# Performance work log

Hardware: AMD Instinct MI355X
Metric: run time of the kernel (lower is better)

The kernel has to match this reference:

```python
import jax, jax.numpy as jnp
import numpy as np

E, H, I, K, T = 32, 2048, 768, 4, 2048


def setup_inputs() -> dict:
    key = jax.random.key(0)
    k1, k2, k3, k4, k5 = jax.random.split(key, 5)
    hidden_states = jax.random.normal(k1, (T, H), dtype=jnp.float32)
    top_k_index = jax.random.randint(k2, (T, K), 0, E, dtype=jnp.int64)
    top_k_weights = jax.random.uniform(k3, (T, K), dtype=jnp.float32)
    gate_up_proj = jax.random.normal(k4, (E, H, 2 * I), dtype=jnp.float32) * 0.02
    down_proj = jax.random.normal(k5, (E, I, H), dtype=jnp.float32) * 0.02
    return {
        "hidden_states": hidden_states,
        "top_k_index": top_k_index,
        "top_k_weights": top_k_weights,
        "gate_up_proj": gate_up_proj,
        "down_proj": down_proj,
    }


def reference(hidden_states, top_k_index, top_k_weights, gate_up_proj, down_proj):
    # Dense routing-weight matrix [T, E]: zeros scattered with top-k weights
    num_tokens = hidden_states.shape[0]
    routing = jnp.zeros((num_tokens, E), dtype=hidden_states.dtype)
    routing = routing.at[jnp.arange(num_tokens)[:, None], top_k_index].set(top_k_weights)

    # Batched (grouped) GEMM over all experts; weights are stored transposed
    # gate_up_proj: [E, H, 2I] -> gu: [E, T, 2I]
    gu = jnp.einsum('th,ehi->eti', hidden_states, gate_up_proj)
    gate, up = jnp.split(gu, 2, axis=-1)           # each [E, T, I]
    inter = jax.nn.silu(gate) * up                 # [E, T, I]
    # down_proj: [E, I, H] -> per-expert output [E, T, H]
    expert_out = jnp.einsum('eti,eih->eth', inter, down_proj)
    # Weighted combine over experts
    out = jnp.einsum('te,eth->th', routing, expert_out)
    return out
```

## Files before the change

### kernel.cpp

```cpp
#include <hip/hip_runtime.h>
#include <hip/hip_bf16.h>

#define E_ 32
#define H_ 2048
#define I_ 768
#define T_ 2048
#define TWO_I 1536
#define MAX_TILES 96

typedef __attribute__((ext_vector_type(8))) short short8;
typedef __attribute__((ext_vector_type(4))) float floatx4;

#define WS_OFFSETS 0
#define WS_IDS     1024
#define WS_WTS     (1024 + 32768)
#define WS_TILES   (1024 + 65536)
#define WS_SLOTTJ  69632
#define WS_INTER   131072
#define WS_HID16   (131072 + 8192*768*2)
#define WS_EO      21102592ULL

__device__ __forceinline__ unsigned short f2bf(float f) {
  union { float f; unsigned u; } v; v.f = f;
  unsigned r = v.u + 0x7FFFu + ((v.u >> 16) & 1u);
  return (unsigned short)(r >> 16);
}

__device__ __forceinline__ unsigned pkbf(float a, float b) {
  __hip_bfloat162 h = __float22bfloat162_rn(float2{a, b});
  union { __hip_bfloat162 h; unsigned u; } v; v.h = h; return v.u;
}

__global__ void build_routing(const int* __restrict__ idx, const float* __restrict__ w,
                              char* __restrict__ ws) {
  int* offs = (int*)(ws + WS_OFFSETS);
  int* ids  = (int*)(ws + WS_IDS);
  float* wt = (float*)(ws + WS_WTS);
  int* tiles = (int*)(ws + WS_TILES);
  int* slot_tj = (int*)(ws + WS_SLOTTJ);
  __shared__ int s_cnt[E_];
  __shared__ int s_pos[E_];
  int tid = threadIdx.x;
  if (tid < E_) s_cnt[tid] = 0;
  __syncthreads();
  for (int i = tid; i < T_ * 4; i += 256) {
    int t = i >> 2, j = i & 3;
    int e = idx[i];
    bool keep = true;
    for (int j2 = j + 1; j2 < 4; ++j2) if (idx[t * 4 + j2] == e) keep = false;
    if (keep) atomicAdd(&s_cnt[e], 1);
  }
  __syncthreads();
  if (tid == 0) {
    int run = 0;
    for (int e = 0; e < E_; ++e) { offs[e] = run; s_pos[e] = run; run += s_cnt[e]; }
    offs[E_] = run;
    int nt = 0;
    for (int e = 0; e < E_; ++e)
      for (int m0 = 0; m0 < s_cnt[e]; m0 += 128) tiles[nt++] = (e << 16) | (m0 >> 7);
    for (; nt < MAX_TILES; ++nt) tiles[nt] = -1;
  }
  __syncthreads();
  for (int i = tid; i < T_ * 4; i += 256) {
    int t = i >> 2, j = i & 3;
    int e = idx[i];
    bool keep = true;
    for (int j2 = j + 1; j2 < 4; ++j2) if (idx[t * 4 + j2] == e) keep = false;
    if (keep) {
      int p = atomicAdd(&s_pos[e], 1);
      ids[p] = t;
      wt[p] = w[i];
      slot_tj[i] = p;
    } else {
      slot_tj[i] = -1;
    }
  }
}

__global__ void cvt_hidden(const float* __restrict__ hs, char* __restrict__ ws) {
  int g = blockIdx.x * 256 + threadIdx.x;
  const float4 f0 = ((const float4*)hs)[g * 2];
  const float4 f1 = ((const float4*)hs)[g * 2 + 1];
  uint4 o;
  o.x = pkbf(f0.x, f0.y); o.y = pkbf(f0.z, f0.w);
  o.z = pkbf(f1.x, f1.y); o.w = pkbf(f1.z, f1.w);
  ((uint4*)(ws + WS_HID16))[g] = o;
}

__global__ __launch_bounds__(256, 2) void gemm1(
    const float* __restrict__ gup, char* __restrict__ ws) {
  const int* offs = (const int*)(ws + WS_OFFSETS);
  const int* ids  = (const int*)(ws + WS_IDS);
  const int* tiles = (const int*)(ws + WS_TILES);
  const unsigned short* h16 = (const unsigned short*)(ws + WS_HID16);
  unsigned short* inter = (unsigned short*)(ws + WS_INTER);

  int tl = tiles[blockIdx.y];
  if (tl < 0) return;
  int e = tl >> 16, m0 = (tl & 0xffff) << 7;
  int start = offs[e];
  int mrem = offs[e + 1] - start - m0;
  int n0 = blockIdx.x * 64;

  __shared__ __align__(16) unsigned short Al[128][72];
  __shared__ __align__(16) unsigned short Bl[128][72];

  int tid = threadIdx.x, lane = tid & 63, wid = tid >> 6;
  int wy = wid >> 1, wx = wid & 1, quad = lane >> 4, l15 = lane & 15;

  floatx4 acc[4][4] = {};

  int arow[4], ako[4];
  const unsigned short* asrc[4];
#pragma unroll
  for (int u = 0; u < 4; ++u) {
    int lin = tid + u * 256;
    arow[u] = lin >> 3; ako[u] = (lin & 7) * 8;
    int tok = (arow[u] < mrem) ? ids[start + m0 + arow[u]] : -1;
    asrc[u] = (tok >= 0) ? h16 + (size_t)tok * H_ + ako[u] : nullptr;
  }
  const float* gB[4];
  int brow0[4], bofs[4];
#pragma unroll
  for (int pp = 0; pp < 4; ++pp) {
    int lin2 = tid + 256 * pp;
    int k2 = lin2 >> 5, c4 = lin2 & 31;
    int gcol = (c4 < 16) ? (n0 + c4 * 4) : (I_ + n0 + (c4 - 16) * 4);
    gB[pp] = gup + (size_t)e * H_ * TWO_I + (size_t)(2 * k2) * TWO_I + gcol;
    brow0[pp] = c4 * 4;
    int chunkp = (k2 >> 2) ^ (c4 & 7);
    bofs[pp] = chunkp * 8 + (k2 & 3) * 2;
  }

  uint4 pf_a[4];
  float4 pf0[4], pf1[4];

  auto loadA = [&](int kb) {
#pragma unroll
    for (int u = 0; u < 4; ++u)
      pf_a[u] = asrc[u] ? *(const uint4*)(asrc[u] + (size_t)kb * 64) : uint4{0u, 0u, 0u, 0u};
  };
  auto loadB = [&](int kb) {
#pragma unroll
    for (int pp = 0; pp < 4; ++pp) {
      const float* p = gB[pp] + (size_t)kb * 64 * TWO_I;
      pf0[pp] = *(const float4*)p;
      pf1[pp] = *(const float4*)(p + TWO_I);
    }
  };

  loadA(0); loadB(0);
  for (int kb = 0; kb < H_ / 64; ++kb) {
#pragma unroll
    for (int u = 0; u < 4; ++u) *(uint4*)&Al[arow[u]][ako[u]] = pf_a[u];
#pragma unroll
    for (int pp = 0; pp < 4; ++pp) {
      *(unsigned*)&Bl[brow0[pp] + 0][bofs[pp]] = pkbf(pf0[pp].x, pf1[pp].x);
      *(unsigned*)&Bl[brow0[pp] + 1][bofs[pp]] = pkbf(pf0[pp].y, pf1[pp].y);
      *(unsigned*)&Bl[brow0[pp] + 2][bofs[pp]] = pkbf(pf0[pp].z, pf1[pp].z);
      *(unsigned*)&Bl[brow0[pp] + 3][bofs[pp]] = pkbf(pf0[pp].w, pf1[pp].w);
    }
    __syncthreads();
    if (kb + 1 < H_ / 64) { loadA(kb + 1); loadB(kb + 1); }
#pragma unroll
    for (int ks = 0; ks < 2; ++ks) {
      short8 af[4], bfr[4];
#pragma unroll
      for (int mi = 0; mi < 4; ++mi)
        af[mi] = *(const short8*)&Al[wy * 64 + mi * 16 + l15][ks * 32 + quad * 8];
#pragma unroll
      for (int ni = 0; ni < 4; ++ni) {
        int j = (ni < 2) ? (wx * 32 + ni * 16 + l15) : (64 + wx * 32 + (ni - 2) * 16 + l15);
        int ch = (ks * 4 + quad) ^ ((j >> 2) & 7);
        bfr[ni] = *(const short8*)&Bl[j][ch * 8];
      }
#pragma unroll
      for (int mi = 0; mi < 4; ++mi)
#pragma unroll
        for (int ni = 0; ni < 4; ++ni)
          acc[mi][ni] = __builtin_amdgcn_mfma_f32_16x16x32_bf16(af[mi], bfr[ni], acc[mi][ni], 0, 0, 0);
    }
    __syncthreads();
  }

#pragma unroll
  for (int mi = 0; mi < 4; ++mi) {
#pragma unroll
    for (int r = 0; r < 4; ++r) {
      int row = wy * 64 + mi * 16 + quad * 4 + r;
      if (row < mrem) {
        int slot = start + m0 + row;
#pragma unroll
        for (int ni = 0; ni < 2; ++ni) {
          float g = acc[mi][ni][r];
          float u = acc[mi][ni + 2][r];
          float s = g / (1.f + __expf(-g));
          int col = n0 + wx * 32 + ni * 16 + l15;
          inter[(size_t)slot * I_ + col] = f2bf(s * u);
        }
      }
    }
  }
}

__global__ __launch_bounds__(256, 2) void gemm2(
    const float* __restrict__ down, char* __restrict__ ws) {
  const int* offs = (const int*)(ws + WS_OFFSETS);
  const float* wt = (const float*)(ws + WS_WTS);
  const int* tiles = (const int*)(ws + WS_TILES);
  const unsigned short* inter = (const unsigned short*)(ws + WS_INTER);
  float* eo = (float*)(ws + WS_EO);

  int tl = tiles[blockIdx.y];
  if (tl < 0) return;
  int e = tl >> 16, m0 = (tl & 0xffff) << 7;
  int start = offs[e];
  int mrem = offs[e + 1] - start - m0;
  int n0 = blockIdx.x * 128;

  __shared__ __align__(16) unsigned short Al[128][72];
  __shared__ __align__(16) unsigned short Bl[128][72];

  int tid = threadIdx.x, lane = tid & 63, wid = tid >> 6;
  int wy = wid >> 1, wx = wid & 1, quad = lane >> 4, l15 = lane & 15;

  floatx4 acc[4][4] = {};

  int arow[4], ako[4];
  const unsigned short* asrc[4];
#pragma unroll
  for (int u = 0; u < 4; ++u) {
    int lin = tid + u * 256;
    arow[u] = lin >> 3; ako[u] = (lin & 7) * 8;
    asrc[u] = (arow[u] < mrem) ? inter + (size_t)(start + m0 + arow[u]) * I_ + ako[u] : nullptr;
  }
  const float* gB[4];
  int brow0[4], bofs[4];
#pragma unroll
  for (int pp = 0; pp < 4; ++pp) {
    int lin2 = tid + 256 * pp;
    int k2 = lin2 >> 5, c4 = lin2 & 31;
    gB[pp] = down + (size_t)e * I_ * H_ + (size_t)(2 * k2) * H_ + (n0 + c4 * 4);
    brow0[pp] = c4 * 4;
    int chunkp = (k2 >> 2) ^ (c4 & 7);
    bofs[pp] = chunkp * 8 + (k2 & 3) * 2;
  }

  uint4 pf_a[4];
  float4 pf0[4], pf1[4];

  auto loadA = [&](int kb) {
#pragma unroll
    for (int u = 0; u < 4; ++u)
      pf_a[u] = asrc[u] ? *(const uint4*)(asrc[u] + (size_t)kb * 64) : uint4{0u, 0u, 0u, 0u};
  };
  auto loadB = [&](int kb) {
#pragma unroll
    for (int pp = 0; pp < 4; ++pp) {
      const float* p = gB[pp] + (size_t)kb * 64 * H_;
      pf0[pp] = *(const float4*)p;
      pf1[pp] = *(const float4*)(p + H_);
    }
  };

  loadA(0); loadB(0);
  for (int kb = 0; kb < I_ / 64; ++kb) {
#pragma unroll
    for (int u = 0; u < 4; ++u) *(uint4*)&Al[arow[u]][ako[u]] = pf_a[u];
#pragma unroll
    for (int pp = 0; pp < 4; ++pp) {
      *(unsigned*)&Bl[brow0[pp] + 0][bofs[pp]] = pkbf(pf0[pp].x, pf1[pp].x);
      *(unsigned*)&Bl[brow0[pp] + 1][bofs[pp]] = pkbf(pf0[pp].y, pf1[pp].y);
      *(unsigned*)&Bl[brow0[pp] + 2][bofs[pp]] = pkbf(pf0[pp].z, pf1[pp].z);
      *(unsigned*)&Bl[brow0[pp] + 3][bofs[pp]] = pkbf(pf0[pp].w, pf1[pp].w);
    }
    __syncthreads();
    if (kb + 1 < I_ / 64) { loadA(kb + 1); loadB(kb + 1); }
#pragma unroll
    for (int ks = 0; ks < 2; ++ks) {
      short8 af[4], bfr[4];
#pragma unroll
      for (int mi = 0; mi < 4; ++mi)
        af[mi] = *(const short8*)&Al[wy * 64 + mi * 16 + l15][ks * 32 + quad * 8];
#pragma unroll
      for (int ni = 0; ni < 4; ++ni) {
        int j = wx * 64 + ni * 16 + l15;
        int ch = (ks * 4 + quad) ^ ((j >> 2) & 7);
        bfr[ni] = *(const short8*)&Bl[j][ch * 8];
      }
#pragma unroll
      for (int mi = 0; mi < 4; ++mi)
#pragma unroll
        for (int ni = 0; ni < 4; ++ni)
          acc[mi][ni] = __builtin_amdgcn_mfma_f32_16x16x32_bf16(af[mi], bfr[ni], acc[mi][ni], 0, 0, 0);
    }
    __syncthreads();
  }

#pragma unroll
  for (int mi = 0; mi < 4; ++mi) {
#pragma unroll
    for (int r = 0; r < 4; ++r) {
      int row = wy * 64 + mi * 16 + quad * 4 + r;
      if (row < mrem) {
        int slot = start + m0 + row;
        float wv = wt[slot];
#pragma unroll
        for (int ni = 0; ni < 4; ++ni) {
          int col = n0 + wx * 64 + ni * 16 + l15;
          eo[(size_t)slot * H_ + col] = wv * acc[mi][ni][r];
        }
      }
    }
  }
}

__global__ void combine(float* __restrict__ out, const char* __restrict__ ws) {
  const int* slot_tj = (const int*)(ws + WS_SLOTTJ);
  const float* eo = (const float*)(ws + WS_EO);
  int g = blockIdx.x * 256 + threadIdx.x;
  int token = g >> 9, c4 = g & 511;
  const int* st = slot_tj + token * 4;
  float4 s = {0.f, 0.f, 0.f, 0.f};
#pragma unroll
  for (int j = 0; j < 4; ++j) {
    int p = st[j];
    if (p >= 0) {
      const float4 v = *(const float4*)(eo + (size_t)p * H_ + c4 * 4);
      s.x += v.x; s.y += v.y; s.z += v.z; s.w += v.w;
    }
  }
  *(float4*)(out + (size_t)token * H_ + c4 * 4) = s;
}

extern "C" void kernel_launch(void* const* d_in, const int* in_sizes, int n_in,
                              void* d_out, int out_size, void* d_ws, size_t ws_size,
                              hipStream_t stream) {
  (void)in_sizes; (void)n_in; (void)out_size; (void)ws_size;
  const float* hidden = (const float*)d_in[0];
  const int* idx      = (const int*)d_in[1];
  const float* w      = (const float*)d_in[2];
  const float* gup    = (const float*)d_in[3];
  const float* down   = (const float*)d_in[4];
  float* out = (float*)d_out;
  char* ws = (char*)d_ws;

  build_routing<<<1, 256, 0, stream>>>(idx, w, ws);
  cvt_hidden<<<T_ * H_ / 8 / 256, 256, 0, stream>>>(hidden, ws);
  gemm1<<<dim3(I_ / 64, MAX_TILES), 256, 0, stream>>>(gup, ws);
  gemm2<<<dim3(H_ / 128, MAX_TILES), 256, 0, stream>>>(down, ws);
  combine<<<T_ * H_ / 4 / 256, 256, 0, stream>>>(out, ws);
}
```

Before: 799.6 us.

## Double-buffer LDS and load A tiles directly to LDS in both GEMMs

```diff
diff --git a/kernel.cpp b/kernel.cpp
--- a/kernel.cpp
+++ b/kernel.cpp
@@ -29,6 +29,12 @@
 __device__ __forceinline__ unsigned pkbf(float a, float b) {
   __hip_bfloat162 h = __float22bfloat162_rn(float2{a, b});
   union { __hip_bfloat162 h; unsigned u; } v; v.h = h; return v.u;
+}
+
+__device__ __forceinline__ void gload_lds16(const unsigned short* g, unsigned short* l) {
+  __builtin_amdgcn_global_load_lds(
+      (__attribute__((address_space(1))) void*)g,
+      (__attribute__((address_space(3))) void*)l, 16, 0, 0);
 }
 
 __global__ void build_routing(const int* __restrict__ idx, const float* __restrict__ w,
@@ -102,22 +108,22 @@
   int mrem = offs[e + 1] - start - m0;
   int n0 = blockIdx.x * 64;
 
-  __shared__ __align__(16) unsigned short Al[128][72];
-  __shared__ __align__(16) unsigned short Bl[128][72];
+  __shared__ __align__(16) unsigned short Al[2][128 * 64];
+  __shared__ __align__(16) unsigned short Bl[2][128][72];
 
   int tid = threadIdx.x, lane = tid & 63, wid = tid >> 6;
   int wy = wid >> 1, wx = wid & 1, quad = lane >> 4, l15 = lane & 15;
 
   floatx4 acc[4][4] = {};
 
-  int arow[4], ako[4];
-  const unsigned short* asrc[4];
+  const unsigned short* aSrc[4];
 #pragma unroll
   for (int u = 0; u < 4; ++u) {
-    int lin = tid + u * 256;
-    arow[u] = lin >> 3; ako[u] = (lin & 7) * 8;
-    int tok = (arow[u] < mrem) ? ids[start + m0 + arow[u]] : -1;
-    asrc[u] = (tok >= 0) ? h16 + (size_t)tok * H_ + ako[u] : nullptr;
+    int s = (wid * 4 + u) * 64 + lane;
+    int r = s >> 3;
+    int c = (s & 7) ^ (r & 7);
+    int tok = ids[start + m0 + ((r < mrem) ? r : 0)];
+    aSrc[u] = h16 + (size_t)tok * H_ + c * 8;
   }
   const float* gB[4];
   int brow0[4], bofs[4];
@@ -128,18 +134,11 @@
     int gcol = (c4 < 16) ? (n0 + c4 * 4) : (I_ + n0 + (c4 - 16) * 4);
     gB[pp] = gup + (size_t)e * H_ * TWO_I + (size_t)(2 * k2) * TWO_I + gcol;
     brow0[pp] = c4 * 4;
-    int chunkp = (k2 >> 2) ^ (c4 & 7);
-    bofs[pp] = chunkp * 8 + (k2 & 3) * 2;
-  }
-
-  uint4 pf_a[4];
+    bofs[pp] = (((k2 >> 2) ^ (c4 & 7)) * 8) + (k2 & 3) * 2;
+  }
+
   float4 pf0[4], pf1[4];
 
-  auto loadA = [&](int kb) {
-#pragma unroll
-    for (int u = 0; u < 4; ++u)
-      pf_a[u] = asrc[u] ? *(const uint4*)(asrc[u] + (size_t)kb * 64) : uint4{0u, 0u, 0u, 0u};
-  };
   auto loadB = [&](int kb) {
 #pragma unroll
     for (int pp = 0; pp < 4; ++pp) {
@@ -148,31 +147,35 @@
       pf1[pp] = *(const float4*)(p + TWO_I);
     }
   };
-
-  loadA(0); loadB(0);
-  for (int kb = 0; kb < H_ / 64; ++kb) {
-#pragma unroll
-    for (int u = 0; u < 4; ++u) *(uint4*)&Al[arow[u]][ako[u]] = pf_a[u];
+  auto stageA = [&](int kb, int buf) {
+#pragma unroll
+    for (int u = 0; u < 4; ++u)
+      gload_lds16(aSrc[u] + kb * 64, &Al[buf][(wid * 4 + u) * 512]);
+  };
+  auto writeB = [&](int buf) {
 #pragma unroll
     for (int pp = 0; pp < 4; ++pp) {
-      *(unsigned*)&Bl[brow0[pp] + 0][bofs[pp]] = pkbf(pf0[pp].x, pf1[pp].x);
-      *(unsigned*)&Bl[brow0[pp] + 1][bofs[pp]] = pkbf(pf0[pp].y, pf1[pp].y);
-      *(unsigned*)&Bl[brow0[pp] + 2][bofs[pp]] = pkbf(pf0[pp].z, pf1[pp].z);
-      *(unsigned*)&Bl[brow0[pp] + 3][bofs[pp]] = pkbf(pf0[pp].w, pf1[pp].w);
-    }
-    __syncthreads();
-    if (kb + 1 < H_ / 64) { loadA(kb + 1); loadB(kb + 1); }
+      *(unsigned*)&Bl[buf][brow0[pp] + 0][bofs[pp]] = pkbf(pf0[pp].x, pf1[pp].x);
+      *(unsigned*)&Bl[buf][brow0[pp] + 1][bofs[pp]] = pkbf(pf0[pp].y, pf1[pp].y);
+      *(unsigned*)&Bl[buf][brow0[pp] + 2][bofs[pp]] = pkbf(pf0[pp].z, pf1[pp].z);
+      *(unsigned*)&Bl[buf][brow0[pp] + 3][bofs[pp]] = pkbf(pf0[pp].w, pf1[pp].w);
+    }
+  };
+  auto compute = [&](int buf) {
 #pragma unroll
     for (int ks = 0; ks < 2; ++ks) {
       short8 af[4], bfr[4];
 #pragma unroll
-      for (int mi = 0; mi < 4; ++mi)
-        af[mi] = *(const short8*)&Al[wy * 64 + mi * 16 + l15][ks * 32 + quad * 8];
+      for (int mi = 0; mi < 4; ++mi) {
+        int row = wy * 64 + mi * 16 + l15;
+        int c16 = (ks * 4 + quad) ^ (row & 7);
+        af[mi] = *(const short8*)&Al[buf][row * 64 + c16 * 8];
+      }
 #pragma unroll
       for (int ni = 0; ni < 4; ++ni) {
         int j = (ni < 2) ? (wx * 32 + ni * 16 + l15) : (64 + wx * 32 + (ni - 2) * 16 + l15);
         int ch = (ks * 4 + quad) ^ ((j >> 2) & 7);
-        bfr[ni] = *(const short8*)&Bl[j][ch * 8];
+        bfr[ni] = *(const short8*)&Bl[buf][j][ch * 8];
       }
 #pragma unroll
       for (int mi = 0; mi < 4; ++mi)
@@ -180,6 +183,23 @@
         for (int ni = 0; ni < 4; ++ni)
           acc[mi][ni] = __builtin_amdgcn_mfma_f32_16x16x32_bf16(af[mi], bfr[ni], acc[mi][ni], 0, 0, 0);
     }
+  };
+
+  const int NK = H_ / 64;
+  loadB(0);
+  stageA(0, 0);
+  writeB(0);
+  __syncthreads();
+
+  for (int kb = 0; kb < NK; ++kb) {
+    int cur = kb & 1, nxt = cur ^ 1;
+    if (kb + 1 < NK) {
+      loadB(kb + 1);
+      stageA(kb + 1, nxt);
+    }
+    compute(cur);
+    __builtin_amdgcn_sched_barrier(0);
+    if (kb + 1 < NK) writeB(nxt);
     __syncthreads();
   }
 
@@ -206,6 +226,7 @@
 __global__ __launch_bounds__(256, 2) void gemm2(
     const float* __restrict__ down, char* __restrict__ ws) {
   const int* offs = (const int*)(ws + WS_OFFSETS);
+  const int* ids  = (const int*)(ws + WS_IDS);
   const float* wt = (const float*)(ws + WS_WTS);
   const int* tiles = (const int*)(ws + WS_TILES);
   const unsigned short* inter = (const unsigned short*)(ws + WS_INTER);
@@ -218,21 +239,22 @@
   int mrem = offs[e + 1] - start - m0;
   int n0 = blockIdx.x * 128;
 
-  __shared__ __align__(16) unsigned short Al[128][72];
-  __shared__ __align__(16) unsigned short Bl[128][72];
+  __shared__ __align__(16) unsigned short Al[2][128 * 64];
+  __shared__ __align__(16) unsigned short Bl[2][128][72];
 
   int tid = threadIdx.x, lane = tid & 63, wid = tid >> 6;
   int wy = wid >> 1, wx = wid & 1, quad = lane >> 4, l15 = lane & 15;
 
   floatx4 acc[4][4] = {};
 
-  int arow[4], ako[4];
-  const unsigned short* asrc[4];
+  const unsigned short* aSrc[4];
 #pragma unroll
   for (int u = 0; u < 4; ++u) {
-    int lin = tid + u * 256;
-    arow[u] = lin >> 3; ako[u] = (lin & 7) * 8;
-    asrc[u] = (arow[u] < mrem) ? inter + (size_t)(start + m0 + arow[u]) * I_ + ako[u] : nullptr;
+    int s = (wid * 4 + u) * 64 + lane;
+    int r = s >> 3;
+    int c = (s & 7) ^ (r & 7);
+    int arow = (r < mrem) ? r : 0;
+    aSrc[u] = inter + (size_t)(start + m0 + arow) * I_ + c * 8;
   }
   const float* gB[4];
   int brow0[4], bofs[4];
@@ -242,18 +264,11 @@
     int k2 = lin2 >> 5, c4 = lin2 & 31;
     gB[pp] = down + (size_t)e * I_ * H_ + (size_t)(2 * k2) * H_ + (n0 + c4 * 4);
     brow0[pp] = c4 * 4;
-    int chunkp = (k2 >> 2) ^ (c4 & 7);
-    bofs[pp] = chunkp * 8 + (k2 & 3) * 2;
-  }
-
-  uint4 pf_a[4];
+    bofs[pp] = (((k2 >> 2) ^ (c4 & 7)) * 8) + (k2 & 3) * 2;
+  }
+
   float4 pf0[4], pf1[4];
 
-  auto loadA = [&](int kb) {
-#pragma unroll
-    for (int u = 0; u < 4; ++u)
-      pf_a[u] = asrc[u] ? *(const uint4*)(asrc[u] + (size_t)kb * 64) : uint4{0u, 0u, 0u, 0u};
-  };
   auto loadB = [&](int kb) {
 #pragma unroll
     for (int pp = 0; pp < 4; ++pp) {
@@ -262,31 +277,35 @@
       pf1[pp] = *(const float4*)(p + H_);
     }
   };
-
-  loadA(0); loadB(0);
-  for (int kb = 0; kb < I_ / 64; ++kb) {
-#pragma unroll
-    for (int u = 0; u < 4; ++u) *(uint4*)&Al[arow[u]][ako[u]] = pf_a[u];
+  auto stageA = [&](int kb, int buf) {
+#pragma unroll
+    for (int u = 0; u < 4; ++u)
+      gload_lds16(aSrc[u] + kb * 64, &Al[buf][(wid * 4 + u) * 512]);
+  };
+  auto writeB = [&](int buf) {
 #pragma unroll
     for (int pp = 0; pp < 4; ++pp) {
-      *(unsigned*)&Bl[brow0[pp] + 0][bofs[pp]] = pkbf(pf0[pp].x, pf1[pp].x);
-      *(unsigned*)&Bl[brow0[pp] + 1][bofs[pp]] = pkbf(pf0[pp].y, pf1[pp].y);
-      *(unsigned*)&Bl[brow0[pp] + 2][bofs[pp]] = pkbf(pf0[pp].z, pf1[pp].z);
-      *(unsigned*)&Bl[brow0[pp] + 3][bofs[pp]] = pkbf(pf0[pp].w, pf1[pp].w);
-    }
-    __syncthreads();
-    if (kb + 1 < I_ / 64) { loadA(kb + 1); loadB(kb + 1); }
+      *(unsigned*)&Bl[buf][brow0[pp] + 0][bofs[pp]] = pkbf(pf0[pp].x, pf1[pp].x);
+      *(unsigned*)&Bl[buf][brow0[pp] + 1][bofs[pp]] = pkbf(pf0[pp].y, pf1[pp].y);
+      *(unsigned*)&Bl[buf][brow0[pp] + 2][bofs[pp]] = pkbf(pf0[pp].z, pf1[pp].z);
+      *(unsigned*)&Bl[buf][brow0[pp] + 3][bofs[pp]] = pkbf(pf0[pp].w, pf1[pp].w);
+    }
+  };
+  auto compute = [&](int buf) {
 #pragma unroll
     for (int ks = 0; ks < 2; ++ks) {
       short8 af[4], bfr[4];
 #pragma unroll
-      for (int mi = 0; mi < 4; ++mi)
-        af[mi] = *(const short8*)&Al[wy * 64 + mi * 16 + l15][ks * 32 + quad * 8];
+      for (int mi = 0; mi < 4; ++mi) {
+        int row = wy * 64 + mi * 16 + l15;
+        int c16 = (ks * 4 + quad) ^ (row & 7);
+        af[mi] = *(const short8*)&Al[buf][row * 64 + c16 * 8];
+      }
 #pragma unroll
       for (int ni = 0; ni < 4; ++ni) {
         int j = wx * 64 + ni * 16 + l15;
         int ch = (ks * 4 + quad) ^ ((j >> 2) & 7);
-        bfr[ni] = *(const short8*)&Bl[j][ch * 8];
+        bfr[ni] = *(const short8*)&Bl[buf][j][ch * 8];
       }
 #pragma unroll
       for (int mi = 0; mi < 4; ++mi)
@@ -294,6 +313,23 @@
         for (int ni = 0; ni < 4; ++ni)
           acc[mi][ni] = __builtin_amdgcn_mfma_f32_16x16x32_bf16(af[mi], bfr[ni], acc[mi][ni], 0, 0, 0);
     }
+  };
+
+  const int NK = I_ / 64;
+  loadB(0);
+  stageA(0, 0);
+  writeB(0);
+  __syncthreads();
+
+  for (int kb = 0; kb < NK; ++kb) {
+    int cur = kb & 1, nxt = cur ^ 1;
+    if (kb + 1 < NK) {
+      loadB(kb + 1);
+      stageA(kb + 1, nxt);
+    }
+    compute(cur);
+    __builtin_amdgcn_sched_barrier(0);
+    if (kb + 1 < NK) writeB(nxt);
     __syncthreads();
   }
 
```

After: 831.6 us. +4.0%, slower.
